# Optimization experiments

Hardware: AMD Instinct MI355X
Metric: run time of the kernel (lower is better)

Reference implementation:

```python
import jax, jax.numpy as jnp
import numpy as np

B, SEQ, PRED = 128, 336, 24
I, H = 64, 256  # input_dim, hidden_dim; bidirectional, num_layers=1


def _lstm_dir(x, h0, c0, Wih, Whh, bih, bhh):
    # x: (B, T, F). torch gate order: i, f, g, o. Returns (hs (B,T,H), h_T, c_T).
    def step(carry, xt):
        h, c = carry
        g = xt @ Wih.T + h @ Whh.T + bih + bhh  # (B, 4H)
        gi, gf, gg, go = jnp.split(g, 4, axis=-1)
        c = jax.nn.sigmoid(gf) * c + jax.nn.sigmoid(gi) * jnp.tanh(gg)
        h = jax.nn.sigmoid(go) * jnp.tanh(c)
        return (h, c), h
    (hT, cT), hs = jax.lax.scan(step, (h0, c0), jnp.swapaxes(x, 0, 1))
    return jnp.swapaxes(hs, 0, 1), hT, cT


def _bilstm(x, h0, c0, Wih, Whh, bih, bhh):
    # h0, c0: (2, B, H) in torch layout [fwd, bwd]; Wih: (2, 4H, F) etc.
    hf, hF, cF = _lstm_dir(x, h0[0], c0[0], Wih[0], Whh[0], bih[0], bhh[0])
    hb, hB, cB = _lstm_dir(x[:, ::-1], h0[1], c0[1], Wih[1], Whh[1], bih[1], bhh[1])
    hb = hb[:, ::-1]
    out = jnp.concatenate([hf, hb], axis=-1)  # (B, T, 2H)
    return out, jnp.stack([hF, hB]), jnp.stack([cF, cB])


def setup_inputs() -> dict:
    key = jax.random.key(0)
    ks = jax.random.split(key, 12)
    s = 0.05
    return {
        "x": jax.random.normal(ks[0], (B, SEQ, I), dtype=jnp.float32),
        "enc_Wih": jax.random.normal(ks[1], (2, 4 * H, I), dtype=jnp.float32) * s,
        "enc_Whh": jax.random.normal(ks[2], (2, 4 * H, H), dtype=jnp.float32) * s,
        "enc_bih": jax.random.normal(ks[3], (2, 4 * H), dtype=jnp.float32) * s,
        "enc_bhh": jax.random.normal(ks[4], (2, 4 * H), dtype=jnp.float32) * s,
        "dec_Wih": jax.random.normal(ks[5], (2, 4 * H, I), dtype=jnp.float32) * s,
        "dec_Whh": jax.random.normal(ks[6], (2, 4 * H, H), dtype=jnp.float32) * s,
        "dec_bih": jax.random.normal(ks[7], (2, 4 * H), dtype=jnp.float32) * s,
        "dec_bhh": jax.random.normal(ks[8], (2, 4 * H), dtype=jnp.float32) * s,
        "lin_W": jax.random.normal(ks[9], (I, 2 * H), dtype=jnp.float32) * s,
        "lin_b": jax.random.normal(ks[10], (I,), dtype=jnp.float32) * s,
    }


def reference(x, enc_Wih, enc_Whh, enc_bih, enc_bhh,
              dec_Wih, dec_Whh, dec_bih, dec_bhh, lin_W, lin_b):
    zeros = jnp.zeros((2, x.shape[0], H), dtype=x.dtype)
    # encoder over full input sequence
    _, h, c = _bilstm(x, zeros, zeros, enc_Wih, enc_Whh, enc_bih, enc_bhh)
    dec_in = x[:, -1:, :]
    outs = []
    for t in range(PRED):
        lstm_out, h, c = _bilstm(dec_in, h, c, dec_Wih, dec_Whh, dec_bih, dec_bhh)
        feat = jnp.concatenate([lstm_out[:, -1, :H], lstm_out[:, 0, H:]], axis=-1)
        y = feat @ lin_W.T + lin_b  # (B, I)
        outs.append(y)
        dec_in = jnp.stack(outs, axis=1)  # (B, t+1, I)
    return jnp.stack(outs, axis=1)  # (B, PRED, I)
```

## Files before the change

kernel.cpp:

```cpp
#include <hip/hip_runtime.h>

#define BB    128
#define SEQL  336
#define PREDN 24
#define IN    64
#define HH    256
#define GG    1024
#define KTOT  320
#define NBLK  256

typedef unsigned int  uint_t;
typedef unsigned short ush;
using s8v = __attribute__((ext_vector_type(8))) short;
using f4v = __attribute__((ext_vector_type(4))) float;

__device__ ush   g_webh[2 * 4 * 256 * KTOT];
__device__ ush   g_webl[2 * 4 * 256 * KTOT];
__device__ ush   g_wdbh[2 * 4 * 256 * KTOT];
__device__ ush   g_wdbl[2 * 4 * 256 * KTOT];
__device__ float g_linwt[2 * HH * IN];
__device__ float g_bs_enc[2 * GG];
__device__ float g_bs_dec[2 * GG];
__device__ float g_linb[IN];
__device__ float g_h[2][2 * BB * HH];
__device__ float g_ys[PREDN * BB * IN];
__device__ int   g_flag[NBLK * 16];

#define N_WT   (2 * 4 * 256 * KTOT)
#define N_PREP (2 * N_WT + 2 * HH * IN + 4 * GG + IN + 2 * 2 * BB * HH + PREDN * BB * IN + NBLK * 16)

__device__ __forceinline__ void bfsplit(float v, uint_t& hi, uint_t& lo) {
    uint_t u = __float_as_uint(v);
    uint_t h = (u + 0x7FFFu + ((u >> 16) & 1u)) >> 16;
    float  r = v - __uint_as_float(h << 16);
    uint_t u2 = __float_as_uint(r);
    uint_t l = (u2 + 0x7FFFu + ((u2 >> 16) & 1u)) >> 16;
    hi = h; lo = l;
}

__global__ void prep_kernel(const float* __restrict__ eWih,
                            const float* __restrict__ eWhh,
                            const float* __restrict__ ebih,
                            const float* __restrict__ ebhh,
                            const float* __restrict__ dWih,
                            const float* __restrict__ dWhh,
                            const float* __restrict__ dbih,
                            const float* __restrict__ dbhh,
                            const float* __restrict__ linW,
                            const float* __restrict__ linb)
{
    int idx = blockIdx.x * 256 + threadIdx.x;
    if (idx >= N_PREP) return;

    if (idx < N_WT) {
        int d   = idx / (4 * 256 * KTOT);
        int sub = idx % (4 * 256 * KTOT);
        int g   = sub / (256 * KTOT);
        int n2  = (sub / KTOT) % 256;
        int k   = sub % KTOT;
        int j   = g * HH + n2;
        float v = (k < IN) ? eWih[(d * GG + j) * IN + k]
                           : eWhh[(d * GG + j) * HH + (k - IN)];
        uint_t hi, lo; bfsplit(v, hi, lo);
        g_webh[idx] = (ush)hi; g_webl[idx] = (ush)lo;
        return;
    }
    idx -= N_WT;
    if (idx < N_WT) {
        int d   = idx / (4 * 256 * KTOT);
        int sub = idx % (4 * 256 * KTOT);
        int g   = sub / (256 * KTOT);
        int n2  = (sub / KTOT) % 256;
        int k   = sub % KTOT;
        int j   = g * HH + n2;
        float v = (k < IN) ? dWih[(d * GG + j) * IN + k]
                           : dWhh[(d * GG + j) * HH + (k - IN)];
        uint_t hi, lo; bfsplit(v, hi, lo);
        g_wdbh[idx] = (ush)hi; g_wdbl[idx] = (ush)lo;
        return;
    }
    idx -= N_WT;
    if (idx < 2 * HH * IN) {
        int k = idx / IN, o = idx % IN;
        g_linwt[idx] = linW[o * (2 * HH) + k];
        return;
    }
    idx -= 2 * HH * IN;
    if (idx < 2 * GG) { g_bs_enc[idx] = ebih[idx] + ebhh[idx]; return; }
    idx -= 2 * GG;
    if (idx < 2 * GG) { g_bs_dec[idx] = dbih[idx] + dbhh[idx]; return; }
    idx -= 2 * GG;
    if (idx < IN) { g_linb[idx] = linb[idx]; return; }
    idx -= IN;
    if (idx < 2 * 2 * BB * HH) { ((float*)g_h)[idx] = 0.0f; return; }
    idx -= 2 * 2 * BB * HH;
    if (idx < PREDN * BB * IN) { g_ys[idx] = 0.0f; return; }
    idx -= PREDN * BB * IN;
    if (idx < NBLK * 16) { g_flag[idx] = 0; return; }
}

__device__ __forceinline__ float sigm(float v) { return 1.0f / (1.0f + expf(-v)); }

__device__ __forceinline__ float agent_ld(const float* p) {
    return __hip_atomic_load(p, __ATOMIC_RELAXED, __HIP_MEMORY_SCOPE_AGENT);
}
__device__ __forceinline__ void agent_st(float* p, float v) {
    __hip_atomic_store(p, v, __ATOMIC_RELAXED, __HIP_MEMORY_SCOPE_AGENT);
}

__global__ __launch_bounds__(256)
void lstm_main(const float* __restrict__ x, float* __restrict__ out)
{
    __shared__ __align__(16) ush  sAh[10 * 64 * 8];
    __shared__ __align__(16) ush  sAl[10 * 64 * 8];
    __shared__ __align__(16) ush  sBh[4 * 10 * 64 * 8];
    __shared__ __align__(16) ush  sBl[4 * 10 * 64 * 8];
    __shared__ float gbuf[4 * 16 * 16];
    __shared__ float um[16 * 516];
    __shared__ float part[16 * 16 * 2];

    const int tid   = threadIdx.x;
    const int blk   = blockIdx.x;
    const int dir   = blk >> 7;
    const int btile = (blk >> 4) & 7;
    const int ntile = blk & 15;
    const int nl    = tid & 15;
    const int bl    = tid >> 4;
    const int n0    = ntile * 16;
    const int b0    = btile * 16;
    const int n     = n0 + nl;
    const int b     = b0 + bl;
    const int lane  = tid & 63;
    const int wave  = tid >> 6;

    int* myflag = &g_flag[blk * 16];
    int  ev = 0;

    auto sync_g = [&](int nwait) {
        ++ev;
        __atomic_signal_fence(__ATOMIC_SEQ_CST);
        __builtin_amdgcn_s_waitcnt(0);
        __atomic_signal_fence(__ATOMIC_SEQ_CST);
        __syncthreads();
        if (tid == 0)
            __hip_atomic_store(myflag, ev, __ATOMIC_RELAXED, __HIP_MEMORY_SCOPE_AGENT);
        if (tid < nwait) {
            int d = (nwait == 32) ? (tid >> 4) : dir;
            int m = tid & 15;
            int* f = &g_flag[(((d << 3) | btile) * 16 + m) * 16];
            while (__hip_atomic_load(f, __ATOMIC_RELAXED, __HIP_MEMORY_SCOPE_AGENT) < ev)
                __builtin_amdgcn_s_sleep(1);
        }
        __atomic_signal_fence(__ATOMIC_SEQ_CST);
        __syncthreads();
    };

    float bw;
    auto load_w = [&](const ush* wh, const ush* wl, const float* bsrc) {
        wh += dir * (4 * 256 * KTOT);
        wl += dir * (4 * 256 * KTOT);
        for (int i = tid; i < 4 * 16 * 80; i += 256) {
            int g   = i / (16 * 80);
            int r   = i % (16 * 80);
            int nl_ = r / 80;
            int k   = (r % 80) * 4;
            int src = ((g * 256) + n0 + nl_) * KTOT + k;
            int kc = k >> 5, quad = (k & 31) >> 3, j = k & 7;
            int dst = ((g * 10 + kc) * 64 + quad * 16 + nl_) * 8 + j;
            *(uint2*)&sBh[dst] = *(const uint2*)(wh + src);
            *(uint2*)&sBl[dst] = *(const uint2*)(wl + src);
        }
        bw = bsrc[dir * GG + wave * HH + n0 + (lane & 15)];
        __syncthreads();
    };

    float c = 0.0f;
    int   p = 0;

    auto step = [&](int mode, int tval, int L) {
        float* hsrc = g_h[p];
        if (mode <= 1) {
            int xb = tid >> 4, xj = tid & 15;
            int te = (mode == 0) ? (dir ? (SEQL - 1 - tval) : tval) : (SEQL - 1);
            float4 xv = ((const float4*)(x + ((b0 + xb) * SEQL + te) * IN))[xj];
            uint_t h0,l0,h1,l1,h2,l2,h3,l3;
            bfsplit(xv.x,h0,l0); bfsplit(xv.y,h1,l1); bfsplit(xv.z,h2,l2); bfsplit(xv.w,h3,l3);
            int k = 4 * xj;
            int base = (((k >> 5) * 64 + ((k & 31) >> 3) * 16 + xb) * 8) + (k & 7);
            *(uint_t*)&sAh[base]     = h0 | (h1 << 16);
            *(uint_t*)&sAh[base + 2] = h2 | (h3 << 16);
            *(uint_t*)&sAl[base]     = l0 | (l1 << 16);
            *(uint_t*)&sAl[base + 2] = l2 | (l3 << 16);
        } else {
            int e = dir ? (L - 1 - tval) : tval;
            float yv[4];
            #pragma unroll
            for (int jj = 0; jj < 4; ++jj) {
                int i = tid + jj * 256;
                yv[jj] = agent_ld(g_ys + (e * BB + b0 + (i >> 6)) * IN + (i & 63));
            }
            #pragma unroll
            for (int jj = 0; jj < 4; ++jj) {
                int i = tid + jj * 256;
                int yb = i >> 6, k = i & 63;
                uint_t hi, lo; bfsplit(yv[jj], hi, lo);
                int base = (((k >> 5) * 64 + ((k & 31) >> 3) * 16 + yb) * 8) + (k & 7);
                sAh[base] = (ush)hi; sAl[base] = (ush)lo;
            }
        }
        {
            int hb = tid & 15, cblk = tid >> 4;
            const float* hp = hsrc + (dir * BB + b0 + hb) * HH + cblk * 16;
            float rh[16];
            #pragma unroll
            for (int m = 0; m < 16; ++m) rh[m] = agent_ld(hp + m);
            #pragma unroll
            for (int m = 0; m < 16; m += 2) {
                int k = IN + cblk * 16 + m;
                uint_t h0,l0,h1,l1;
                bfsplit(rh[m], h0, l0); bfsplit(rh[m+1], h1, l1);
                int base = (((k >> 5) * 64 + ((k & 31) >> 3) * 16 + hb) * 8) + (k & 7);
                *(uint_t*)&sAh[base] = h0 | (h1 << 16);
                *(uint_t*)&sAl[base] = l0 | (l1 << 16);
            }
        }
        __syncthreads();

        f4v acc = { bw, bw, bw, bw };
        const s8v* pAh = (const s8v*)sAh;
        const s8v* pAl = (const s8v*)sAl;
        const s8v* pBh = (const s8v*)sBh + wave * 10 * 64;
        const s8v* pBl = (const s8v*)sBl + wave * 10 * 64;
        #pragma unroll
        for (int kc = 0; kc < 10; ++kc) {
            s8v ah = pAh[kc * 64 + lane];
            s8v al = pAl[kc * 64 + lane];
            s8v bh = pBh[kc * 64 + lane];
            s8v blo = pBl[kc * 64 + lane];
            acc = __builtin_amdgcn_mfma_f32_16x16x32_bf16(ah, bh,  acc, 0, 0, 0);
            acc = __builtin_amdgcn_mfma_f32_16x16x32_bf16(ah, blo, acc, 0, 0, 0);
            acc = __builtin_amdgcn_mfma_f32_16x16x32_bf16(al, bh,  acc, 0, 0, 0);
        }
        {
            int quad = lane >> 4, ncol = lane & 15;
            #pragma unroll
            for (int r2 = 0; r2 < 4; ++r2)
                gbuf[(wave * 16 + quad * 4 + r2) * 16 + ncol] = acc[r2];
        }
        __syncthreads();
        {
            float gi_ = gbuf[(0 * 16 + bl) * 16 + nl];
            float gf_ = gbuf[(1 * 16 + bl) * 16 + nl];
            float gg_ = gbuf[(2 * 16 + bl) * 16 + nl];
            float go_ = gbuf[(3 * 16 + bl) * 16 + nl];
            c = sigm(gf_) * c + sigm(gi_) * tanhf(gg_);
            float hn = sigm(go_) * tanhf(c);
            agent_st(&g_h[p ^ 1][(dir * BB + b) * HH + n], hn);
        }
        p ^= 1;
    };

    load_w(g_webh, g_webl, g_bs_enc);
    for (int t = 0; t < SEQL; ++t) { step(0, t, 0); sync_g(16); }

    load_w(g_wdbh, g_wdbl, g_bs_dec);

    for (int t = 0; t < PREDN; ++t) {
        int L = t ? t : 1;
        for (int s = 0; s < L; ++s) {
            step((t == 0) ? 1 : 2, s, L);
            sync_g((s == L - 1) ? 32 : 16);
        }
        {
            float* hc = g_h[p];
            float rh2[32];
            #pragma unroll
            for (int jj = 0; jj < 32; ++jj) {
                int i = tid + jj * 256;
                int bl2 = i >> 9, j = i & 511;
                const float* base = (j < 256) ? (hc + (b0 + bl2) * HH + j)
                                              : (hc + (BB + b0 + bl2) * HH + (j - 256));
                rh2[jj] = agent_ld(base);
            }
            #pragma unroll
            for (int jj = 0; jj < 32; ++jj) {
                int i = tid + jj * 256;
                int bl2 = i >> 9, j = i & 511;
                um[bl2 * 516 + j] = rh2[jj];
            }
            __syncthreads();
            int bl2 = tid >> 4, ks = tid & 15;
            int o0  = ((dir << 4) | ntile) << 1;
            float p0 = 0.0f, p1 = 0.0f;
            const float* hr = &um[bl2 * 516 + ks * 32];
            const float* lw = g_linwt + (ks * 32) * IN + o0;
            #pragma unroll 8
            for (int j = 0; j < 32; ++j) {
                float hv = hr[j];
                p0 = fmaf(hv, lw[j * IN],     p0);
                p1 = fmaf(hv, lw[j * IN + 1], p1);
            }
            part[(bl2 * 16 + ks) * 2]     = p0;
            part[(bl2 * 16 + ks) * 2 + 1] = p1;
            __syncthreads();
            if (tid < 32) {
                int b2 = tid >> 1, oi = tid & 1;
                float acc2 = g_linb[o0 + oi];
                #pragma unroll
                for (int m2 = 0; m2 < 16; ++m2) acc2 += part[(b2 * 16 + m2) * 2 + oi];
                agent_st(&g_ys[(t * BB + b0 + b2) * IN + o0 + oi], acc2);
                out[(b0 + b2) * (PREDN * IN) + t * IN + o0 + oi] = acc2;
            }
            sync_g(32);
        }
    }
}

extern "C" void kernel_launch(void* const* d_in, const int* in_sizes, int n_in,
                              void* d_out, int out_size, void* d_ws, size_t ws_size,
                              hipStream_t stream)
{
    (void)in_sizes; (void)n_in; (void)out_size; (void)d_ws; (void)ws_size;
    const float* x    = (const float*)d_in[0];
    const float* eWih = (const float*)d_in[1];
    const float* eWhh = (const float*)d_in[2];
    const float* ebih = (const float*)d_in[3];
    const float* ebhh = (const float*)d_in[4];
    const float* dWih = (const float*)d_in[5];
    const float* dWhh = (const float*)d_in[6];
    const float* dbih = (const float*)d_in[7];
    const float* dbhh = (const float*)d_in[8];
    const float* linW = (const float*)d_in[9];
    const float* linb = (const float*)d_in[10];
    float* out = (float*)d_out;

    int prep_blocks = (N_PREP + 255) / 256;
    hipLaunchKernelGGL(prep_kernel, dim3(prep_blocks), dim3(256), 0, stream,
                       eWih, eWhh, ebih, ebhh, dWih, dWhh, dbih, dbhh, linW, linb);

    void* args[] = { (void*)&x, (void*)&out };
    (void)hipLaunchCooperativeKernel((void*)lstm_main, dim3(NBLK), dim3(256), args, 0, stream);
}
```

Measured before the change: 3.413 ms.

## Shrink grid to 64 blocks with register-resident weights and single-block head

Repartitions the persistent LSTM so each block owns 64 hidden columns across all four gates (64 blocks instead of 256), keeping the bf16 hi/lo weight slices in registers rather than shared memory. The gate nonlinearity is computed straight from the MFMA accumulators, which removes the gbuf round trip and a block barrier. Each step's grid sync now waits on only 4 peers (8 on the final step of a decode round) instead of 16 or 32. The linear head runs on 8 blocks from a dedicated final-hidden buffer, and the launch switches from cooperative to a plain launch, which relies on all 64 blocks being co-resident. In exchange, per-block MFMA work per step roughly quadruples and register pressure becomes very high.

Result: slower. 5.101 ms (+49.4%).

```diff
diff --git a/kernel.cpp b/kernel.cpp
--- a/kernel.cpp
+++ b/kernel.cpp
@@ -7,9 +7,9 @@
 #define HH    256
 #define GG    1024
 #define KTOT  320
-#define NBLK  256
-
-typedef unsigned int  uint_t;
+#define NBLK  64
+
+typedef unsigned int   uint_t;
 typedef unsigned short ush;
 using s8v = __attribute__((ext_vector_type(8))) short;
 using f4v = __attribute__((ext_vector_type(4))) float;
@@ -24,6 +24,7 @@
 __device__ float g_linb[IN];
 __device__ float g_h[2][2 * BB * HH];
 __device__ float g_ys[PREDN * BB * IN];
+__device__ float g_hfin[PREDN * 8 * 8192];
 __device__ int   g_flag[NBLK * 16];
 
 #define N_WT   (2 * 4 * 256 * KTOT)
@@ -107,31 +108,31 @@
 __device__ __forceinline__ void agent_st(float* p, float v) {
     __hip_atomic_store(p, v, __ATOMIC_RELAXED, __HIP_MEMORY_SCOPE_AGENT);
 }
-
-__global__ __launch_bounds__(256)
+__device__ __forceinline__ int agent_ldi(const int* p) {
+    return __hip_atomic_load(p, __ATOMIC_RELAXED, __HIP_MEMORY_SCOPE_AGENT);
+}
+__device__ __forceinline__ void agent_sti(int* p, int v) {
+    __hip_atomic_store(p, v, __ATOMIC_RELAXED, __HIP_MEMORY_SCOPE_AGENT);
+}
+
+__global__ __launch_bounds__(256, 1)
 void lstm_main(const float* __restrict__ x, float* __restrict__ out)
 {
     __shared__ __align__(16) ush  sAh[10 * 64 * 8];
     __shared__ __align__(16) ush  sAl[10 * 64 * 8];
-    __shared__ __align__(16) ush  sBh[4 * 10 * 64 * 8];
-    __shared__ __align__(16) ush  sBl[4 * 10 * 64 * 8];
-    __shared__ float gbuf[4 * 16 * 16];
-    __shared__ float um[16 * 516];
-    __shared__ float part[16 * 16 * 2];
+    __shared__ float umf[16][513];
 
     const int tid   = threadIdx.x;
     const int blk   = blockIdx.x;
-    const int dir   = blk >> 7;
-    const int btile = (blk >> 4) & 7;
-    const int ntile = blk & 15;
-    const int nl    = tid & 15;
-    const int bl    = tid >> 4;
-    const int n0    = ntile * 16;
+    const int dir   = blk >> 5;
+    const int q     = (blk >> 3) & 3;
+    const int btile = blk & 7;
     const int b0    = btile * 16;
-    const int n     = n0 + nl;
-    const int b     = b0 + bl;
+    const int wave  = tid >> 6;
     const int lane  = tid & 63;
-    const int wave  = tid >> 6;
+    const int quad  = lane >> 4;
+    const int n16   = lane & 15;
+    const int colG  = q * 64 + wave * 16 + n16;
 
     int* myflag = &g_flag[blk * 16];
     int  ev = 0;
@@ -142,42 +143,36 @@
         __builtin_amdgcn_s_waitcnt(0);
         __atomic_signal_fence(__ATOMIC_SEQ_CST);
         __syncthreads();
-        if (tid == 0)
-            __hip_atomic_store(myflag, ev, __ATOMIC_RELAXED, __HIP_MEMORY_SCOPE_AGENT);
+        if (tid == 0) agent_sti(myflag, ev);
         if (tid < nwait) {
-            int d = (nwait == 32) ? (tid >> 4) : dir;
-            int m = tid & 15;
-            int* f = &g_flag[(((d << 3) | btile) * 16 + m) * 16];
-            while (__hip_atomic_load(f, __ATOMIC_RELAXED, __HIP_MEMORY_SCOPE_AGENT) < ev)
-                __builtin_amdgcn_s_sleep(1);
+            int d = (nwait == 8) ? (tid >> 2) : dir;
+            int m = (nwait == 8) ? (tid & 3) : tid;
+            int* f = &g_flag[(d * 32 + m * 8 + btile) * 16];
+            while (agent_ldi(f) < ev) __builtin_amdgcn_s_sleep(1);
         }
         __atomic_signal_fence(__ATOMIC_SEQ_CST);
         __syncthreads();
     };
 
-    float bw;
+    s8v   rbh[4][10], rbl[4][10];
+    float bw[4];
     auto load_w = [&](const ush* wh, const ush* wl, const float* bsrc) {
-        wh += dir * (4 * 256 * KTOT);
-        wl += dir * (4 * 256 * KTOT);
-        for (int i = tid; i < 4 * 16 * 80; i += 256) {
-            int g   = i / (16 * 80);
-            int r   = i % (16 * 80);
-            int nl_ = r / 80;
-            int k   = (r % 80) * 4;
-            int src = ((g * 256) + n0 + nl_) * KTOT + k;
-            int kc = k >> 5, quad = (k & 31) >> 3, j = k & 7;
-            int dst = ((g * 10 + kc) * 64 + quad * 16 + nl_) * 8 + j;
-            *(uint2*)&sBh[dst] = *(const uint2*)(wh + src);
-            *(uint2*)&sBl[dst] = *(const uint2*)(wl + src);
-        }
-        bw = bsrc[dir * GG + wave * HH + n0 + (lane & 15)];
-        __syncthreads();
+        #pragma unroll
+        for (int g4 = 0; g4 < 4; ++g4) {
+            #pragma unroll
+            for (int kc = 0; kc < 10; ++kc) {
+                int src = ((dir * 4 + g4) * 256 + colG) * KTOT + kc * 32 + quad * 8;
+                rbh[g4][kc] = *(const s8v*)(wh + src);
+                rbl[g4][kc] = *(const s8v*)(wl + src);
+            }
+            bw[g4] = bsrc[dir * GG + g4 * 256 + colG];
+        }
     };
 
-    float c = 0.0f;
+    float cst[4] = {0.0f, 0.0f, 0.0f, 0.0f};
     int   p = 0;
 
-    auto step = [&](int mode, int tval, int L) {
+    auto step = [&](int mode, int tval, int L, int fin_t) {
         float* hsrc = g_h[p];
         if (mode <= 1) {
             int xb = tid >> 4, xj = tid & 15;
@@ -226,93 +221,87 @@
         }
         __syncthreads();
 
-        f4v acc = { bw, bw, bw, bw };
+        f4v a0 = {bw[0], bw[0], bw[0], bw[0]};
+        f4v a1 = {bw[1], bw[1], bw[1], bw[1]};
+        f4v a2 = {bw[2], bw[2], bw[2], bw[2]};
+        f4v a3 = {bw[3], bw[3], bw[3], bw[3]};
         const s8v* pAh = (const s8v*)sAh;
         const s8v* pAl = (const s8v*)sAl;
-        const s8v* pBh = (const s8v*)sBh + wave * 10 * 64;
-        const s8v* pBl = (const s8v*)sBl + wave * 10 * 64;
         #pragma unroll
         for (int kc = 0; kc < 10; ++kc) {
             s8v ah = pAh[kc * 64 + lane];
             s8v al = pAl[kc * 64 + lane];
-            s8v bh = pBh[kc * 64 + lane];
-            s8v blo = pBl[kc * 64 + lane];
-            acc = __builtin_amdgcn_mfma_f32_16x16x32_bf16(ah, bh,  acc, 0, 0, 0);
-            acc = __builtin_amdgcn_mfma_f32_16x16x32_bf16(ah, blo, acc, 0, 0, 0);
-            acc = __builtin_amdgcn_mfma_f32_16x16x32_bf16(al, bh,  acc, 0, 0, 0);
-        }
+            a0 = __builtin_amdgcn_mfma_f32_16x16x32_bf16(ah, rbh[0][kc], a0, 0, 0, 0);
+            a0 = __builtin_amdgcn_mfma_f32_16x16x32_bf16(ah, rbl[0][kc], a0, 0, 0, 0);
+            a0 = __builtin_amdgcn_mfma_f32_16x16x32_bf16(al, rbh[0][kc], a0, 0, 0, 0);
+            a1 = __builtin_amdgcn_mfma_f32_16x16x32_bf16(ah, rbh[1][kc], a1, 0, 0, 0);
+            a1 = __builtin_amdgcn_mfma_f32_16x16x32_bf16(ah, rbl[1][kc], a1, 0, 0, 0);
+            a1 = __builtin_amdgcn_mfma_f32_16x16x32_bf16(al, rbh[1][kc], a1, 0, 0, 0);
+            a2 = __builtin_amdgcn_mfma_f32_16x16x32_bf16(ah, rbh[2][kc], a2, 0, 0, 0);
+            a2 = __builtin_amdgcn_mfma_f32_16x16x32_bf16(ah, rbl[2][kc], a2, 0, 0, 0);
+            a2 = __builtin_amdgcn_mfma_f32_16x16x32_bf16(al, rbh[2][kc], a2, 0, 0, 0);
+            a3 = __builtin_amdgcn_mfma_f32_16x16x32_bf16(ah, rbh[3][kc], a3, 0, 0, 0);
+            a3 = __builtin_amdgcn_mfma_f32_16x16x32_bf16(ah, rbl[3][kc], a3, 0, 0, 0);
+            a3 = __builtin_amdgcn_mfma_f32_16x16x32_bf16(al, rbh[3][kc], a3, 0, 0, 0);
+        }
+
         {
-            int quad = lane >> 4, ncol = lane & 15;
-            #pragma unroll
-            for (int r2 = 0; r2 < 4; ++r2)
-                gbuf[(wave * 16 + quad * 4 + r2) * 16 + ncol] = acc[r2];
-        }
-        __syncthreads();
-        {
-            float gi_ = gbuf[(0 * 16 + bl) * 16 + nl];
-            float gf_ = gbuf[(1 * 16 + bl) * 16 + nl];
-            float gg_ = gbuf[(2 * 16 + bl) * 16 + nl];
-            float go_ = gbuf[(3 * 16 + bl) * 16 + nl];
-            c = sigm(gf_) * c + sigm(gi_) * tanhf(gg_);
-            float hn = sigm(go_) * tanhf(c);
-            agent_st(&g_h[p ^ 1][(dir * BB + b) * HH + n], hn);
+            float* hdst = g_h[p ^ 1];
+            #pragma unroll
+            for (int r2 = 0; r2 < 4; ++r2) {
+                float gi = a0[r2], gf = a1[r2], gg2 = a2[r2], go = a3[r2];
+                cst[r2] = sigm(gf) * cst[r2] + sigm(gi) * tanhf(gg2);
+                float hn = sigm(go) * tanhf(cst[r2]);
+                int row = quad * 4 + r2;
+                agent_st(&hdst[(dir * BB + b0 + row) * HH + colG], hn);
+                if (fin_t >= 0)
+                    agent_st(&g_hfin[(fin_t * 8 + btile) * 8192
+                                     + (dir * HH + colG) * 16 + row], hn);
+            }
         }
         p ^= 1;
+        sync_g((fin_t >= 0) ? 8 : 4);
     };
 
+    auto head = [&](int t) {
+        if (blk < 8) {
+            #pragma unroll
+            for (int jj = 0; jj < 32; ++jj) {
+                int gi = tid + jj * 256;
+                umf[gi & 15][gi >> 4] =
+                    agent_ld(&g_hfin[(t * 8 + btile) * 8192 + gi]);
+            }
+            __syncthreads();
+            int row = tid >> 4, og = tid & 15;
+            float acc[4];
+            #pragma unroll
+            for (int oi = 0; oi < 4; ++oi) acc[oi] = g_linb[og * 4 + oi];
+            for (int k2 = 0; k2 < 512; ++k2) {
+                float hv = umf[row][k2];
+                #pragma unroll
+                for (int oi = 0; oi < 4; ++oi)
+                    acc[oi] = fmaf(hv, g_linwt[k2 * IN + og * 4 + oi], acc[oi]);
+            }
+            #pragma unroll
+            for (int oi = 0; oi < 4; ++oi) {
+                int o = og * 4 + oi;
+                out[(b0 + row) * (PREDN * IN) + t * IN + o] = acc[oi];
+                agent_st(&g_ys[(t * BB + b0 + row) * IN + o], acc[oi]);
+            }
+        }
+        sync_g(8);
+    };
+
     load_w(g_webh, g_webl, g_bs_enc);
-    for (int t = 0; t < SEQL; ++t) { step(0, t, 0); sync_g(16); }
+    for (int t = 0; t < SEQL; ++t) step(0, t, 0, -1);
 
     load_w(g_wdbh, g_wdbl, g_bs_dec);
 
     for (int t = 0; t < PREDN; ++t) {
         int L = t ? t : 1;
-        for (int s = 0; s < L; ++s) {
-            step((t == 0) ? 1 : 2, s, L);
-            sync_g((s == L - 1) ? 32 : 16);
-        }
-        {
-            float* hc = g_h[p];
-            float rh2[32];
-            #pragma unroll
-            for (int jj = 0; jj < 32; ++jj) {
-                int i = tid + jj * 256;
-                int bl2 = i >> 9, j = i & 511;
-                const float* base = (j < 256) ? (hc + (b0 + bl2) * HH + j)
-                                              : (hc + (BB + b0 + bl2) * HH + (j - 256));
-                rh2[jj] = agent_ld(base);
-            }
-            #pragma unroll
-            for (int jj = 0; jj < 32; ++jj) {
-                int i = tid + jj * 256;
-                int bl2 = i >> 9, j = i & 511;
-                um[bl2 * 516 + j] = rh2[jj];
-            }
-            __syncthreads();
-            int bl2 = tid >> 4, ks = tid & 15;
-            int o0  = ((dir << 4) | ntile) << 1;
-            float p0 = 0.0f, p1 = 0.0f;
-            const float* hr = &um[bl2 * 516 + ks * 32];
-            const float* lw = g_linwt + (ks * 32) * IN + o0;
-            #pragma unroll 8
-            for (int j = 0; j < 32; ++j) {
-                float hv = hr[j];
-                p0 = fmaf(hv, lw[j * IN],     p0);
-                p1 = fmaf(hv, lw[j * IN + 1], p1);
-            }
-            part[(bl2 * 16 + ks) * 2]     = p0;
-            part[(bl2 * 16 + ks) * 2 + 1] = p1;
-            __syncthreads();
-            if (tid < 32) {
-                int b2 = tid >> 1, oi = tid & 1;
-                float acc2 = g_linb[o0 + oi];
-                #pragma unroll
-                for (int m2 = 0; m2 < 16; ++m2) acc2 += part[(b2 * 16 + m2) * 2 + oi];
-                agent_st(&g_ys[(t * BB + b0 + b2) * IN + o0 + oi], acc2);
-                out[(b0 + b2) * (PREDN * IN) + t * IN + o0 + oi] = acc2;
-            }
-            sync_g(32);
-        }
+        for (int s = 0; s < L; ++s)
+            step((t == 0) ? 1 : 2, s, L, (s == L - 1) ? t : -1);
+        head(t);
     }
 }
 
@@ -338,6 +327,5 @@
     hipLaunchKernelGGL(prep_kernel, dim3(prep_blocks), dim3(256), 0, stream,
                        eWih, eWhh, ebih, ebhh, dWih, dWhh, dbih, dbhh, linW, linb);
 
-    void* args[] = { (void*)&x, (void*)&out };
-    (void)hipLaunchCooperativeKernel((void*)lstm_main, dim3(NBLK), dim3(256), args, 0, stream);
-}
+    hipLaunchKernelGGL(lstm_main, dim3(NBLK), dim3(256), 0, stream, x, out);
+}
```
